# Optimization experiments

Measured on AMD Instinct MI355X. Metric: run time of the kernel, lower is better.

## Reference

```python
import jax, jax.numpy as jnp
import numpy as np
from jax import lax

B, H, W = 2, 128, 128
C_FEAT, DIM_LOI, DIM_FC = 256, 128, 1024
N_PTS0, N_PTS1 = 32, 8
L_LINES = 16384
TOPK = 300            # n_dyn_junc
JUNC_TH = 0.008       # junc_thresh
IMG_W, IMG_H = 512.0, 512.0  # annotation width/height -> sx=sy=4


def setup_inputs() -> dict:
    key = jax.random.key(0)
    ks = jax.random.split(key, 12)
    s = 0.02
    return {
        "output": jax.random.normal(ks[0], (B, 9, H, W), jnp.float32),
        "features": jax.random.normal(ks[1], (B, C_FEAT, H, W), jnp.float32),
        "line_preds": jax.random.uniform(ks[2], (B, L_LINES, 4), jnp.float32) * (W - 1),
        "conv_w": jax.random.normal(ks[3], (DIM_LOI, C_FEAT), jnp.float32) * s,
        "conv_b": jax.random.normal(ks[4], (DIM_LOI,), jnp.float32) * s,
        "w1": jax.random.normal(ks[5], (DIM_LOI * N_PTS1, DIM_FC), jnp.float32) * s,
        "b1": jax.random.normal(ks[6], (DIM_FC,), jnp.float32) * s,
        "w2": jax.random.normal(ks[7], (DIM_FC, DIM_FC), jnp.float32) * s,
        "b2": jax.random.normal(ks[8], (DIM_FC,), jnp.float32) * s,
        "w3": jax.random.normal(ks[9], (DIM_FC, 1), jnp.float32) * s,
        "b3": jax.random.normal(ks[10], (1,), jnp.float32) * s,
    }


def _nms2d(a):
    # F.max_pool2d(a, 3, stride=1, padding=1); keep only local maxima
    ap = lax.reduce_window(a, -jnp.inf, lax.max, (3, 3), (1, 1), "SAME")
    return a * (a == ap).astype(a.dtype)


def _get_junctions(jloc_nms, joff):
    # jloc_nms: [H,W]; joff: [2,H,W]
    flat = jloc_nms.reshape(-1)
    scores, idx = lax.top_k(flat, TOPK)            # [J]
    joff_f = joff.reshape(2, -1)
    y = (idx // W).astype(jnp.float32) + joff_f[1][idx] + 0.5
    x = (idx % W).astype(jnp.float32) + joff_f[0][idx] + 0.5
    juncs = jnp.stack([x, y], axis=-1)             # [J,2]
    valid = scores > JUNC_TH
    juncs = jnp.where(valid[:, None], juncs, 1e6)
    return juncs, valid


def _pool_lines(feat, lines, w1, b1, w2, b2, w3, b3):
    # feat: [C,H,W]; lines: [L,4] (x1,y1,x2,y2)
    C = feat.shape[0]
    L = lines.shape[0]
    t = jnp.linspace(0.0, 1.0, N_PTS0)                       # tspan
    start, end = lines[:, :2], lines[:, 2:]
    # [L, n_pts0, 2] sample points along each line
    pts = start[:, None, :] * t[None, :, None] + end[:, None, :] * (1.0 - t)[None, :, None] - 0.5
    px = pts[..., 0].reshape(-1)
    py = pts[..., 1].reshape(-1)
    px0 = jnp.clip(jnp.floor(px), 0.0, W - 1.0)
    py0 = jnp.clip(jnp.floor(py), 0.0, H - 1.0)
    px1 = jnp.clip(px0 + 1.0, 0.0, W - 1.0)
    py1 = jnp.clip(py0 + 1.0, 0.0, H - 1.0)
    x0, y0 = px0.astype(jnp.int32), py0.astype(jnp.int32)
    x1, y1 = px1.astype(jnp.int32), py1.astype(jnp.int32)
    f2 = feat.reshape(C, H * W)

    def g(yi, xi):
        return f2[:, yi * W + xi]                             # [C, L*n_pts0]

    xp = (g(y0, x0) * (py1 - py) * (px1 - px)
          + g(y1, x0) * (py - py0) * (px1 - px)
          + g(y0, x1) * (py1 - py) * (px - px0)
          + g(y1, x1) * (py - py0) * (px - px0))
    xp = xp.reshape(C, L, N_PTS0).transpose(1, 0, 2)          # [L, C, n_pts0]
    # MaxPool1d(kernel=n_pts0//n_pts1, stride same)
    xp = xp.reshape(L, C, N_PTS1, N_PTS0 // N_PTS1).max(-1)   # [L, C, n_pts1]
    xp = xp.reshape(L, C * N_PTS1)
    h = jax.nn.relu(xp @ w1 + b1)
    h = jax.nn.relu(h @ w2 + b2)
    return (h @ w3 + b3).ravel()                              # [L]


def _per_image(out9, loi_feat, lines_prop, w1, b1, w2, b2, w3, b3):
    jloc = jax.nn.softmax(out9[5:7], axis=0)[1]               # [H,W]
    joff = jax.nn.sigmoid(out9[7:9]) - 0.5                    # [2,H,W]
    juncs, _ = _get_junctions(_nms2d(jloc), joff)             # [J,2]
    # nearest junction to each line endpoint
    d1 = jnp.sum((lines_prop[None, :, :2] - juncs[:, None]) ** 2, axis=-1)  # [J,L]
    d2 = jnp.sum((lines_prop[None, :, 2:] - juncs[:, None]) ** 2, axis=-1)
    i1 = jnp.argmin(d1, axis=0)
    i2 = jnp.argmin(d2, axis=0)
    imin = jnp.minimum(i1, i2)
    imax = jnp.maximum(i1, i2)
    iskeep = imin < imax                                      # drop degenerate
    lines = jnp.concatenate([juncs[imin], juncs[imax]], axis=1)  # [L,4]
    logits = _pool_lines(loi_feat, lines, w1, b1, w2, b2, w3, b3)
    scores = jax.nn.sigmoid(logits)
    keep = iskeep & (scores > 0.05)
    sx = IMG_W / W
    sy = IMG_H / H
    lines2 = lines.reshape(-1, 2, 2) * jnp.array([sx, sy], jnp.float32)
    return lines2, scores, keep


def reference(output, features, line_preds, conv_w, conv_b, w1, b1, w2, b2, w3, b3):
    # 1x1 conv: dim_feat -> dim_loi
    loi = jnp.einsum("bchw,dc->bdhw", features, conv_w) + conv_b[None, :, None, None]
    fn = lambda o, f, lp: _per_image(o, f, lp, w1, b1, w2, b2, w3, b3)
    lines, scores, keep = jax.vmap(fn)(output, loi, line_preds)
    return lines, scores, keep
```

## Files before the change

kernel.cpp:

```cpp
#include <hip/hip_runtime.h>
#include <hip/hip_bf16.h>
#include <cstdint>
#include <cstddef>

#define HW     16384
#define WIDTH  128
#define NB     2
#define NTOPK  300
#define JUNC_TH 0.008f

typedef __attribute__((ext_vector_type(8))) short s16x8;
typedef __attribute__((ext_vector_type(2))) float f32x2;
typedef __attribute__((ext_vector_type(4))) float f32x4;
typedef __attribute__((ext_vector_type(4))) int   i32x4;
typedef __attribute__((ext_vector_type(8))) int   i32x8;

__device__ __forceinline__ float sigm(float x) { return 1.0f / (1.0f + expf(-x)); }

__device__ __forceinline__ unsigned short f2bf(float f) {
  __hip_bfloat16 h = __float2bfloat16(f);
  return __hip_bfloat16_raw(h).x;
}
__device__ __forceinline__ unsigned char f2fp8(float v) {
  return (unsigned char)(__builtin_amdgcn_cvt_pk_fp8_f32(v, 0.0f, 0, false) & 0xff);
}
__device__ __forceinline__ f32x2 bfpair(unsigned int u) {
  f32x2 r;
  r[0] = __uint_as_float(u << 16);
  r[1] = __uint_as_float(u & 0xffff0000u);
  return r;
}
__device__ __forceinline__ f32x2 pkmul(f32x2 a, f32x2 b) {
  f32x2 d;
  asm("v_pk_mul_f32 %0, %1, %2" : "=v"(d) : "v"(a), "v"(b));
  return d;
}
__device__ __forceinline__ f32x2 pkadd(f32x2 a, f32x2 b) {
  f32x2 d;
  asm("v_pk_add_f32 %0, %1, %2" : "=v"(d) : "v"(a), "v"(b));
  return d;
}
__device__ __forceinline__ f32x2 max2(f32x2 a, f32x2 b) {
  f32x2 r;
  r[0] = fmaxf(a[0], b[0]);
  r[1] = fmaxf(a[1], b[1]);
  return r;
}

#define GLOAD_LDS16(gp, lp)                                                        \
  __builtin_amdgcn_global_load_lds((const __attribute__((address_space(1))) void*)(gp), \
                                   (__attribute__((address_space(3))) void*)(lp), 16, 0, 0)

__device__ __forceinline__ void fc_tile_map(int bid, int nm, int& m_idx, int& n_idx) {
  if ((nm & 7) == 0) {
    int x = bid & 7;
    int k = bid >> 3;
    m_idx = x * (nm >> 3) + (k >> 2);
    n_idx = k & 3;
  } else {
    m_idx = bid >> 2;
    n_idx = bid & 3;
  }
}

__global__ void k_transpose_w(const float* __restrict__ w, float* __restrict__ wt) {
  int i = blockIdx.x * 256 + threadIdx.x;
  int d = i & 127, c = i >> 7;
  wt[c * 128 + d] = w[d * 256 + c];
}

__global__ __launch_bounds__(256) void k_wtrans(const float* __restrict__ w,
                                                unsigned char* __restrict__ wt) {
  __shared__ float tile[32][33];
  int n0 = blockIdx.x * 32, k0 = blockIdx.y * 32;
  int tx = threadIdx.x & 31, ty = threadIdx.x >> 5;
#pragma unroll
  for (int r = 0; r < 32; r += 8)
    tile[ty + r][tx] = w[(size_t)(k0 + ty + r) * 1024 + n0 + tx];
  __syncthreads();
#pragma unroll
  for (int r = 0; r < 32; r += 8)
    wt[(size_t)(n0 + ty + r) * 1024 + k0 + tx] = f2fp8(tile[tx][ty + r]);
}

__global__ __launch_bounds__(256) void k_loi(const float* __restrict__ F,
                                             const float* __restrict__ wt,
                                             const float* __restrict__ bias,
                                             unsigned short* __restrict__ loi) {
  int b = blockIdx.y;
  int p0 = blockIdx.x * 64;
  __shared__ float As[8][64];
  __shared__ float Bs[8][128];
  int t = threadIdx.x;
  int tn = t & 15;
  int tm = t >> 4;
  float acc[4][8];
#pragma unroll
  for (int i = 0; i < 4; ++i)
#pragma unroll
    for (int j = 0; j < 8; ++j) acc[i][j] = 0.0f;

  const float* Fb = F + (size_t)b * 256 * HW;
  for (int c0 = 0; c0 < 256; c0 += 8) {
    __syncthreads();
    if (t < 128) {
      int kk = t >> 4, mv = t & 15;
      float4 v = *(const float4*)(Fb + (size_t)(c0 + kk) * HW + p0 + mv * 4);
      *(float4*)&As[kk][mv * 4] = v;
    }
    {
      int kk = t >> 5, dv = t & 31;
      float4 v = *(const float4*)(wt + (size_t)(c0 + kk) * 128 + dv * 4);
      *(float4*)&Bs[kk][dv * 4] = v;
    }
    __syncthreads();
#pragma unroll
    for (int kk = 0; kk < 8; ++kk) {
      float4 a4 = *(const float4*)&As[kk][tm * 4];
      float4 b0 = *(const float4*)&Bs[kk][tn * 8];
      float4 b1 = *(const float4*)&Bs[kk][tn * 8 + 4];
      float av[4] = {a4.x, a4.y, a4.z, a4.w};
      float bv[8] = {b0.x, b0.y, b0.z, b0.w, b1.x, b1.y, b1.z, b1.w};
#pragma unroll
      for (int i = 0; i < 4; ++i)
#pragma unroll
        for (int j = 0; j < 8; ++j) acc[i][j] += av[i] * bv[j];
    }
  }
  float4 c0v = *(const float4*)(bias + tn * 8);
  float4 c1v = *(const float4*)(bias + tn * 8 + 4);
  float bb[8] = {c0v.x, c0v.y, c0v.z, c0v.w, c1v.x, c1v.y, c1v.z, c1v.w};
#pragma unroll
  for (int i = 0; i < 4; ++i) {
    int p = p0 + tm * 4 + i;
    alignas(16) unsigned short o[8];
#pragma unroll
    for (int j = 0; j < 8; ++j) o[j] = f2bf(acc[i][j] + bb[j]);
    *(s16x8*)(loi + ((size_t)b * HW + p) * 128 + tn * 8) = *(const s16x8*)o;
  }
}

__global__ void k_jloc(const float* __restrict__ out9, float* __restrict__ jloc) {
  int i = blockIdx.x * 256 + threadIdx.x;
  int b = i >> 14, p = i & (HW - 1);
  const float* base = out9 + (size_t)b * 9 * HW;
  float o5 = base[5 * HW + p], o6 = base[6 * HW + p];
  float m = fmaxf(o5, o6);
  float e5 = expf(o5 - m), e6 = expf(o6 - m);
  jloc[i] = e6 / (e5 + e6);
}

__global__ void k_nmskey(const float* __restrict__ jloc, unsigned long long* __restrict__ keys) {
  int i = blockIdx.x * 256 + threadIdx.x;
  int b = i >> 14, p = i & (HW - 1);
  int y = p >> 7, x = p & 127;
  const float* J = jloc + (size_t)b * HW;
  float c = J[p];
  float m = c;
  for (int dy = -1; dy <= 1; ++dy) {
    int yy = y + dy;
    if (yy < 0 || yy > 127) continue;
    for (int dx = -1; dx <= 1; ++dx) {
      int xx = x + dx;
      if (xx < 0 || xx > 127) continue;
      m = fmaxf(m, J[yy * WIDTH + xx]);
    }
  }
  unsigned int vb = (c == m) ? __float_as_uint(c) : 0u;
  keys[i] = ((unsigned long long)vb << 32) | (unsigned int)(~p);
}

__global__ __launch_bounds__(1024) void k_topk(const unsigned long long* __restrict__ keys,
                                               const float* __restrict__ out9,
                                               float* __restrict__ jx, float* __restrict__ jy) {
  int b = blockIdx.x;
  __shared__ unsigned long long cand[4096];
  __shared__ int cnt;
  int t = threadIdx.x;
  if (t == 0) cnt = 0;
#pragma unroll
  for (int i = t; i < 4096; i += 1024) cand[i] = 0ull;
  __syncthreads();
  const unsigned long long* K = keys + (size_t)b * HW;
  for (int i = t; i < HW; i += 1024) {
    unsigned long long k = K[i];
    if ((k >> 32) != 0ull) {
      int pos = atomicAdd(&cnt, 1);
      if (pos < 4096) cand[pos] = k;
    }
  }
  __syncthreads();
  for (int k = 2; k <= 4096; k <<= 1) {
    for (int j = k >> 1; j > 0; j >>= 1) {
#pragma unroll
      for (int idx = t; idx < 4096; idx += 1024) {
        int ixj = idx ^ j;
        if (ixj > idx) {
          unsigned long long a = cand[idx], c = cand[ixj];
          bool up = ((idx & k) == 0);
          if (up ? (a < c) : (a > c)) { cand[idx] = c; cand[ixj] = a; }
        }
      }
      __syncthreads();
    }
  }
  if (t < NTOPK) {
    const float* o7 = out9 + (size_t)b * 9 * HW + 7 * HW;
    const float* o8 = out9 + (size_t)b * 9 * HW + 8 * HW;
    unsigned long long bb = cand[t];
    unsigned int vb = (unsigned int)(bb >> 32);
    float val = __uint_as_float(vb);
    if (vb != 0u && val > JUNC_TH) {
      int p = (int)(~((unsigned int)(bb & 0xffffffffull))) & (HW - 1);
      float ox = sigm(o7[p]) - 0.5f;
      float oy = sigm(o8[p]) - 0.5f;
      jx[b * NTOPK + t] = (float)(p & 127) + ox + 0.5f;
      jy[b * NTOPK + t] = (float)(p >> 7) + oy + 0.5f;
    } else {
      jx[b * NTOPK + t] = 1000000.0f;
      jy[b * NTOPK + t] = 1000000.0f;
    }
  }
}

__global__ __launch_bounds__(256) void k_lines(const float* __restrict__ lp,
                                               const float* __restrict__ jx,
                                               const float* __restrict__ jy,
                                               float4* __restrict__ lines4,
                                               int* __restrict__ iskeep,
                                               float* __restrict__ out_lines) {
  int b = blockIdx.y;
  int l = blockIdx.x * 256 + threadIdx.x;
  __shared__ float jxs[NTOPK], jys[NTOPK];
  for (int i = threadIdx.x; i < NTOPK; i += 256) {
    jxs[i] = jx[b * NTOPK + i];
    jys[i] = jy[b * NTOPK + i];
  }
  __syncthreads();
  int gl = b * HW + l;
  const float* L = lp + (size_t)gl * 4;
  float x1 = L[0], y1 = L[1], x2 = L[2], y2 = L[3];
  float bd1 = 3.4e38f, bd2 = 3.4e38f;
  int i1 = 0, i2 = 0;
  for (int j = 0; j < NTOPK; ++j) {
    float ax = __fsub_rn(x1, jxs[j]);
    float ay = __fsub_rn(y1, jys[j]);
    float d1 = __fadd_rn(__fmul_rn(ax, ax), __fmul_rn(ay, ay));
    if (d1 < bd1) { bd1 = d1; i1 = j; }
    float ex = __fsub_rn(x2, jxs[j]);
    float ey = __fsub_rn(y2, jys[j]);
    float d2 = __fadd_rn(__fmul_rn(ex, ex), __fmul_rn(ey, ey));
    if (d2 < bd2) { bd2 = d2; i2 = j; }
  }
  int imin = min(i1, i2), imax = max(i1, i2);
  float sx1 = jxs[imin], sy1 = jys[imin], sx2 = jxs[imax], sy2 = jys[imax];
  lines4[gl] = make_float4(sx1, sy1, sx2, sy2);
  iskeep[gl] = (imin < imax) ? 1 : 0;
  ((float4*)out_lines)[gl] = make_float4(sx1 * 4.0f, sy1 * 4.0f, sx2 * 4.0f, sy2 * 4.0f);
}

__global__ __launch_bounds__(128) void k_sample(const unsigned short* __restrict__ loi,
                                                const float4* __restrict__ lines4,
                                                unsigned char* __restrict__ xvec,
                                                int b_base, int l0, int rows_per_b) {
  __shared__ __align__(16) int   soff[2][32][4];
  __shared__ __align__(16) f32x2 swt2[2][32][4];
  int b = b_base + blockIdx.y;
  int t = threadIdx.x;
  if (t < 64) {
    int li = t >> 5, k = t & 31;
    int l = l0 + blockIdx.x * 2 + li;
    float4 ln = lines4[b * HW + l];
    float tt = (float)k * (1.0f / 31.0f);
    float tc = 1.0f - tt;
    float px = ln.x * tt + ln.z * tc - 0.5f;
    float py = ln.y * tt + ln.w * tc - 0.5f;
    float px0 = fminf(fmaxf(floorf(px), 0.0f), 127.0f);
    float py0 = fminf(fmaxf(floorf(py), 0.0f), 127.0f);
    float px1 = fminf(px0 + 1.0f, 127.0f);
    float py1 = fminf(py0 + 1.0f, 127.0f);
    int ix0 = (int)px0, iy0 = (int)py0, ix1 = (int)px1, iy1 = (int)py1;
    float wy1 = __fsub_rn(py1, py), wy0 = __fsub_rn(py, py0);
    float wx1 = __fsub_rn(px1, px), wx0 = __fsub_rn(px, px0);
    soff[li][k][0] = (iy0 * WIDTH + ix0) * 128;
    soff[li][k][1] = (iy1 * WIDTH + ix0) * 128;
    soff[li][k][2] = (iy0 * WIDTH + ix1) * 128;
    soff[li][k][3] = (iy1 * WIDTH + ix1) * 128;
    float wa = __fmul_rn(wy1, wx1);
    float wb = __fmul_rn(wy0, wx1);
    float wc = __fmul_rn(wy1, wx0);
    float wd = __fmul_rn(wy0, wx0);
    swt2[li][k][0] = (f32x2){wa, wa};
    swt2[li][k][1] = (f32x2){wb, wb};
    swt2[li][k][2] = (f32x2){wc, wc};
    swt2[li][k][3] = (f32x2){wd, wd};
  }
  __syncthreads();
  int li = t >> 6, c2 = t & 63;
  int l = l0 + blockIdx.x * 2 + li;
  const unsigned short* Lb = loi + (size_t)b * HW * 128 + (c2 << 1);
  f32x2 rm = (f32x2){-3.4e38f, -3.4e38f};
  f32x2 fv2[8];
#pragma unroll 4
  for (int k = 0; k < 32; ++k) {
    int4  o   = *(const int4*)soff[li][k];
    f32x4 w01 = *(const f32x4*)&swt2[li][k][0];
    f32x4 w23 = *(const f32x4*)&swt2[li][k][2];
    f32x2 wa; wa[0] = w01[0]; wa[1] = w01[1];
    f32x2 wb; wb[0] = w01[2]; wb[1] = w01[3];
    f32x2 wc; wc[0] = w23[0]; wc[1] = w23[1];
    f32x2 wd; wd[0] = w23[2]; wd[1] = w23[3];
    unsigned int u0 = *(const unsigned int*)(Lb + o.x);
    unsigned int u1 = *(const unsigned int*)(Lb + o.y);
    unsigned int u2 = *(const unsigned int*)(Lb + o.z);
    unsigned int u3 = *(const unsigned int*)(Lb + o.w);
    f32x2 s = pkadd(pkadd(pkadd(pkmul(bfpair(u0), wa), pkmul(bfpair(u1), wb)),
                          pkmul(bfpair(u2), wc)), pkmul(bfpair(u3), wd));
    rm = max2(rm, s);
    if ((k & 3) == 3) {
      fv2[k >> 2] = rm;
      rm = (f32x2){-3.4e38f, -3.4e38f};
    }
  }
  int4 pk;
  int d;
  d = __builtin_amdgcn_cvt_pk_fp8_f32(fv2[0][0], fv2[1][0], 0, false);
  d = __builtin_amdgcn_cvt_pk_fp8_f32(fv2[2][0], fv2[3][0], d, true);
  pk.x = d;
  d = __builtin_amdgcn_cvt_pk_fp8_f32(fv2[4][0], fv2[5][0], 0, false);
  d = __builtin_amdgcn_cvt_pk_fp8_f32(fv2[6][0], fv2[7][0], d, true);
  pk.y = d;
  d = __builtin_amdgcn_cvt_pk_fp8_f32(fv2[0][1], fv2[1][1], 0, false);
  d = __builtin_amdgcn_cvt_pk_fp8_f32(fv2[2][1], fv2[3][1], d, true);
  pk.z = d;
  d = __builtin_amdgcn_cvt_pk_fp8_f32(fv2[4][1], fv2[5][1], 0, false);
  d = __builtin_amdgcn_cvt_pk_fp8_f32(fv2[6][1], fv2[7][1], d, true);
  pk.w = d;
  size_t xrow = (size_t)blockIdx.y * rows_per_b + (l - l0);
  *(int4*)(xvec + xrow * 1024 + c2 * 16) = pk;
}

#define ACC_COLS(X, mi) X(mi,0) X(mi,1) X(mi,2) X(mi,3) X(mi,4) X(mi,5) X(mi,6) X(mi,7)
#define ACC_ALL(X) ACC_COLS(X,0) ACC_COLS(X,1) ACC_COLS(X,2) ACC_COLS(X,3)
#define MXMFMA(a, b, c) \
  __builtin_amdgcn_mfma_scale_f32_16x16x128_f8f6f4(a, b, c, 0, 0, 0, 0x7f7f7f7f, 0, 0x7f7f7f7f)

__device__ __forceinline__ i32x8 ldf(const unsigned char* p, int s0, int s1) {
  i32x4 lo = *(const i32x4*)(p + s0);
  i32x4 hi = *(const i32x4*)(p + s1);
  i32x8 r;
  r[0] = lo[0]; r[1] = lo[1]; r[2] = lo[2]; r[3] = lo[3];
  r[4] = hi[0]; r[5] = hi[1]; r[6] = hi[2]; r[7] = hi[3];
  return r;
}

template <int MODE>
__global__ __launch_bounds__(512, 1) void k_fc(const unsigned char* __restrict__ A,
                                               const unsigned char* __restrict__ Bt,
                                               const float* __restrict__ bias,
                                               unsigned char* __restrict__ C,
                                               const float* __restrict__ w3,
                                               float* __restrict__ logp,
                                               int base, int nm) {
  __shared__ __align__(16) unsigned char sm[131072];
  int t = threadIdx.x, lane = t & 63, w = t >> 6;
  int wm = w & 3, wn = w >> 2;
  int lr = lane & 15, ls = lane >> 4;
  int m_idx, n_idx;
  fc_tile_map(blockIdx.x, nm, m_idx, n_idx);
  int m0 = m_idx * 256, n0 = n_idx * 256;

  int srow = t >> 3;
  int cst = (t & 7) ^ (srow & 7);
  const unsigned char* gA = A + (size_t)(m0 + srow) * 1024 + cst * 16;
  const unsigned char* gB = Bt + (size_t)(n0 + srow) * 1024 + cst * 16;
  unsigned char* sdst = sm + t * 16;

  int s0 = ((2 * ls) ^ (lr & 7)) * 16;
  int s1 = ((2 * ls + 1) ^ (lr & 7)) * 16;
  int aoff = (wm * 64 + lr) * 128;
  int boff = 32768 + (wn * 128 + lr) * 128;

#define DECLC(mi, ni) f32x4 c##mi##ni = (f32x4){0.f, 0.f, 0.f, 0.f};
  ACC_ALL(DECLC)
#undef DECLC

#pragma unroll
  for (int q = 0; q < 4; ++q) GLOAD_LDS16(gA + (size_t)q * 65536, sdst + q * 8192);
#pragma unroll
  for (int q = 0; q < 4; ++q) GLOAD_LDS16(gB + (size_t)q * 65536, sdst + 32768 + q * 8192);
  __syncthreads();

#pragma unroll 2
  for (int it = 0; it < 8; ++it) {
    int cur = it & 1;
    if (it < 7) {
      int kb = (it + 1) * 128;
      unsigned char* d = sdst + (cur ^ 1) * 65536;
#pragma unroll
      for (int q = 0; q < 4; ++q) GLOAD_LDS16(gA + kb + (size_t)q * 65536, d + q * 8192);
#pragma unroll
      for (int q = 0; q < 4; ++q) GLOAD_LDS16(gB + kb + (size_t)q * 65536, d + 32768 + q * 8192);
    }
    const unsigned char* T = sm + cur * 65536;
    const unsigned char* TA = T + aoff;
    const unsigned char* TB = T + boff;
    i32x8 a0 = ldf(TA, s0, s1);
    i32x8 a1 = ldf(TA + 2048, s0, s1);
    i32x8 a2 = ldf(TA + 4096, s0, s1);
    i32x8 a3 = ldf(TA + 6144, s0, s1);
#define DO_NI(ni)                                    \
    {                                                \
      i32x8 b_ = ldf(TB + ni * 2048, s0, s1);        \
      c0##ni = MXMFMA(a0, b_, c0##ni);               \
      c1##ni = MXMFMA(a1, b_, c1##ni);               \
      c2##ni = MXMFMA(a2, b_, c2##ni);               \
      c3##ni = MXMFMA(a3, b_, c3##ni);               \
    }
    DO_NI(0) DO_NI(1) DO_NI(2) DO_NI(3) DO_NI(4) DO_NI(5) DO_NI(6) DO_NI(7)
#undef DO_NI
    __syncthreads();
  }

#define DECLBV(ni) float bv##ni = bias[n0 + wn * 128 + ni * 16 + lr];
  DECLBV(0) DECLBV(1) DECLBV(2) DECLBV(3) DECLBV(4) DECLBV(5) DECLBV(6) DECLBV(7)
#undef DECLBV

  if constexpr (MODE == 0) {
    __syncthreads();
#define EPI(mi, ni)                                                          \
    {                                                                        \
      int cl = wn * 128 + ni * 16 + lr;                                      \
      int rl = wm * 64 + mi * 16 + ls * 4;                                   \
      sm[(rl + 0) * 272 + cl] = f2fp8(fmaxf(c##mi##ni[0] + bv##ni, 0.0f));   \
      sm[(rl + 1) * 272 + cl] = f2fp8(fmaxf(c##mi##ni[1] + bv##ni, 0.0f));   \
      sm[(rl + 2) * 272 + cl] = f2fp8(fmaxf(c##mi##ni[2] + bv##ni, 0.0f));   \
      sm[(rl + 3) * 272 + cl] = f2fp8(fmaxf(c##mi##ni[3] + bv##ni, 0.0f));   \
    }
    ACC_ALL(EPI)
#undef EPI
    __syncthreads();
#pragma unroll
    for (int p = 0; p < 8; ++p) {
      int row = p * 32 + (t >> 4), seg = t & 15;
      *(int4*)(C + (size_t)(m0 + row) * 1024 + n0 + seg * 16) =
          *(const int4*)(sm + row * 272 + seg * 16);
    }
  } else {
#define DECLWV(ni) float wv##ni = w3[n0 + wn * 128 + ni * 16 + lr];
    DECLWV(0) DECLWV(1) DECLWV(2) DECLWV(3) DECLWV(4) DECLWV(5) DECLWV(6) DECLWV(7)
#undef DECLWV
    f32x4 pm0 = (f32x4){0.f, 0.f, 0.f, 0.f}, pm1 = pm0, pm2 = pm0, pm3 = pm0;
#define RED(mi, ni)                                                   \
    {                                                                 \
      pm##mi[0] += fmaxf(c##mi##ni[0] + bv##ni, 0.0f) * wv##ni;       \
      pm##mi[1] += fmaxf(c##mi##ni[1] + bv##ni, 0.0f) * wv##ni;       \
      pm##mi[2] += fmaxf(c##mi##ni[2] + bv##ni, 0.0f) * wv##ni;       \
      pm##mi[3] += fmaxf(c##mi##ni[3] + bv##ni, 0.0f) * wv##ni;       \
    }
    ACC_ALL(RED)
#undef RED
    __syncthreads();
    float* red = (float*)sm;
#define SHF(mi, r)                                                    \
    {                                                                 \
      float v = pm##mi[r];                                            \
      v += __shfl_xor(v, 1, 64);                                      \
      v += __shfl_xor(v, 2, 64);                                      \
      v += __shfl_xor(v, 4, 64);                                      \
      v += __shfl_xor(v, 8, 64);                                      \
      if (lr == 0) red[(wm * 64 + mi * 16 + ls * 4 + r) * 2 + wn] = v; \
    }
    SHF(0, 0) SHF(0, 1) SHF(0, 2) SHF(0, 3)
    SHF(1, 0) SHF(1, 1) SHF(1, 2) SHF(1, 3)
    SHF(2, 0) SHF(2, 1) SHF(2, 2) SHF(2, 3)
    SHF(3, 0) SHF(3, 1) SHF(3, 2) SHF(3, 3)
#undef SHF
    __syncthreads();
    if (t < 256)
      logp[(size_t)(base + m0 + t) * 4 + n_idx] = red[t * 2] + red[t * 2 + 1];
  }
}

__global__ __launch_bounds__(256) void k_fin(const float* __restrict__ logp,
                                             const float* __restrict__ b3,
                                             const int* __restrict__ iskeep,
                                             float* __restrict__ oscore,
                                             float* __restrict__ okeep,
                                             int base) {
  int gl = base + blockIdx.x * 256 + threadIdx.x;
  float4 a = ((const float4*)logp)[gl];
  float s = (a.x + a.y) + (a.z + a.w);
  float sc = sigm(s + b3[0]);
  oscore[gl] = sc;
  okeep[gl] = (iskeep[gl] && sc > 0.05f) ? 1.0f : 0.0f;
}

extern "C" void kernel_launch(void* const* d_in, const int* in_sizes, int n_in,
                              void* d_out, int out_size, void* d_ws, size_t ws_size,
                              hipStream_t stream) {
  const float* output     = (const float*)d_in[0];
  const float* features   = (const float*)d_in[1];
  const float* line_preds = (const float*)d_in[2];
  const float* conv_w     = (const float*)d_in[3];
  const float* conv_b     = (const float*)d_in[4];
  const float* w1         = (const float*)d_in[5];
  const float* b1         = (const float*)d_in[6];
  const float* w2         = (const float*)d_in[7];
  const float* b2         = (const float*)d_in[8];
  const float* w3         = (const float*)d_in[9];
  const float* b3         = (const float*)d_in[10];

  char* ws = (char*)d_ws;
  size_t off = 0;
  auto alloc = [&](size_t bytes) -> void* {
    void* p = ws + off;
    off += (bytes + 255) & ~(size_t)255;
    return p;
  };
  float* wt      = (float*)alloc((size_t)256 * 128 * 4);
  unsigned short* loi = (unsigned short*)alloc((size_t)NB * HW * 128 * 2);
  float* jloc    = (float*)alloc((size_t)NB * HW * 4);
  unsigned long long* keys = (unsigned long long*)alloc((size_t)NB * HW * 8);
  float* jx      = (float*)alloc((size_t)NB * NTOPK * 4);
  float* jy      = (float*)alloc((size_t)NB * NTOPK * 4);
  float4* lines4 = (float4*)alloc((size_t)NB * HW * 16);
  int* iskeep    = (int*)alloc((size_t)NB * HW * 4);
  float* logp    = (float*)alloc((size_t)NB * HW * 4 * 4);
  unsigned char* w1b = (unsigned char*)alloc((size_t)1024 * 1024);
  unsigned char* w2b = (unsigned char*)alloc((size_t)1024 * 1024);
  size_t fixed = off;

  bool merged = (fixed + (size_t)2 * NB * HW * 1024 + 512 <= ws_size);
  int CH = 256;
  if (!merged) {
    const int cands[7] = {16384, 8192, 4096, 2048, 1024, 512, 256};
    for (int ci = 0; ci < 7; ++ci) {
      if (fixed + (size_t)2 * cands[ci] * 1024 + 512 <= ws_size) { CH = cands[ci]; break; }
    }
  }
  size_t actrows = merged ? (size_t)NB * HW : (size_t)CH;
  unsigned char* xvec = (unsigned char*)alloc(actrows * 1024);
  unsigned char* h1   = (unsigned char*)alloc(actrows * 1024);

  float* out_lines  = (float*)d_out;
  float* out_scores = out_lines + (size_t)NB * HW * 4;
  float* out_keep   = out_scores + (size_t)NB * HW;

  k_transpose_w<<<128, 256, 0, stream>>>(conv_w, wt);
  k_wtrans<<<dim3(32, 32), 256, 0, stream>>>(w1, w1b);
  k_wtrans<<<dim3(32, 32), 256, 0, stream>>>(w2, w2b);
  k_loi<<<dim3(HW / 64, NB), 256, 0, stream>>>(features, wt, conv_b, loi);
  k_jloc<<<NB * HW / 256, 256, 0, stream>>>(output, jloc);
  k_nmskey<<<NB * HW / 256, 256, 0, stream>>>(jloc, keys);
  k_topk<<<NB, 1024, 0, stream>>>(keys, output, jx, jy);
  k_lines<<<dim3(HW / 256, NB), 256, 0, stream>>>(line_preds, jx, jy, lines4, iskeep, out_lines);

  if (merged) {
    int M = NB * HW, nm = M / 256;
    k_sample<<<dim3(HW / 2, NB), 128, 0, stream>>>(loi, lines4, xvec, 0, 0, HW);
    k_fc<0><<<nm * 4, 512, 0, stream>>>(xvec, w1b, b1, h1, nullptr, nullptr, 0, nm);
    k_fc<1><<<nm * 4, 512, 0, stream>>>(h1, w2b, b2, nullptr, w3, logp, 0, nm);
    k_fin<<<M / 256, 256, 0, stream>>>(logp, b3, iskeep, out_scores, out_keep, 0);
  } else {
    int nchunk = HW / CH, nm = CH / 256;
    for (int b = 0; b < NB; ++b) {
      for (int ci = 0; ci < nchunk; ++ci) {
        int l0 = ci * CH;
        int base = b * HW + l0;
        k_sample<<<dim3(CH / 2, 1), 128, 0, stream>>>(loi, lines4, xvec, b, l0, CH);
        k_fc<0><<<nm * 4, 512, 0, stream>>>(xvec, w1b, b1, h1, nullptr, nullptr, 0, nm);
        k_fc<1><<<nm * 4, 512, 0, stream>>>(h1, w2b, b2, nullptr, w3, logp, base, nm);
        k_fin<<<CH / 256, 256, 0, stream>>>(logp, b3, iskeep, out_scores, out_keep, base);
      }
    }
  }
}
```

Before: 333.2 us.

## Compute 1x1 conv projection with bf16 MFMA instead of scalar FMA

Rewrites the k_loi 1x1-convolution GEMM so that features and weights are converted to bf16 while staged in shared memory, and the products run on the MFMA 16x16x32 bf16 instruction with fp32 accumulation. The K step grows from 8 to 32 channels per iteration. This removes the scalar FP32 FMA loop. In exchange it lowers input precision to bf16, and the transposed staging uses scalar shared-memory stores plus narrow 2-byte scattered output writes.

```diff
diff --git a/kernel.cpp b/kernel.cpp
--- a/kernel.cpp
+++ b/kernel.cpp
@@ -87,56 +87,72 @@
                                              const float* __restrict__ wt,
                                              const float* __restrict__ bias,
                                              unsigned short* __restrict__ loi) {
+  __shared__ __align__(16) unsigned short Ash[64 * 40];
+  __shared__ __align__(16) unsigned short Bsh[128 * 40];
   int b = blockIdx.y;
   int p0 = blockIdx.x * 64;
-  __shared__ float As[8][64];
-  __shared__ float Bs[8][128];
   int t = threadIdx.x;
-  int tn = t & 15;
-  int tm = t >> 4;
-  float acc[4][8];
-#pragma unroll
-  for (int i = 0; i < 4; ++i)
-#pragma unroll
-    for (int j = 0; j < 8; ++j) acc[i][j] = 0.0f;
-
+  int wv = t >> 6, lane = t & 63;
+  int lr = lane & 15, ls = lane >> 4;
   const float* Fb = F + (size_t)b * 256 * HW;
-  for (int c0 = 0; c0 < 256; c0 += 8) {
-    __syncthreads();
-    if (t < 128) {
-      int kk = t >> 4, mv = t & 15;
-      float4 v = *(const float4*)(Fb + (size_t)(c0 + kk) * HW + p0 + mv * 4);
-      *(float4*)&As[kk][mv * 4] = v;
-    }
-    {
-      int kk = t >> 5, dv = t & 31;
-      float4 v = *(const float4*)(wt + (size_t)(c0 + kk) * 128 + dv * 4);
-      *(float4*)&Bs[kk][dv * 4] = v;
-    }
-    __syncthreads();
-#pragma unroll
-    for (int kk = 0; kk < 8; ++kk) {
-      float4 a4 = *(const float4*)&As[kk][tm * 4];
-      float4 b0 = *(const float4*)&Bs[kk][tn * 8];
-      float4 b1 = *(const float4*)&Bs[kk][tn * 8 + 4];
-      float av[4] = {a4.x, a4.y, a4.z, a4.w};
-      float bv[8] = {b0.x, b0.y, b0.z, b0.w, b1.x, b1.y, b1.z, b1.w};
-#pragma unroll
-      for (int i = 0; i < 4; ++i)
-#pragma unroll
-        for (int j = 0; j < 8; ++j) acc[i][j] += av[i] * bv[j];
-    }
-  }
-  float4 c0v = *(const float4*)(bias + tn * 8);
-  float4 c1v = *(const float4*)(bias + tn * 8 + 4);
-  float bb[8] = {c0v.x, c0v.y, c0v.z, c0v.w, c1v.x, c1v.y, c1v.z, c1v.w};
-#pragma unroll
-  for (int i = 0; i < 4; ++i) {
-    int p = p0 + tm * 4 + i;
-    alignas(16) unsigned short o[8];
-#pragma unroll
-    for (int j = 0; j < 8; ++j) o[j] = f2bf(acc[i][j] + bb[j]);
-    *(s16x8*)(loi + ((size_t)b * HW + p) * 128 + tn * 8) = *(const s16x8*)o;
+
+  f32x4 acc[8];
+#pragma unroll
+  for (int dg = 0; dg < 8; ++dg) acc[dg] = (f32x4){0.f, 0.f, 0.f, 0.f};
+
+  int cc = t >> 3, pg = t & 7;
+
+  for (int c0 = 0; c0 < 256; c0 += 32) {
+    const float* fr = Fb + (size_t)(c0 + cc) * HW + p0 + pg * 8;
+    float4 fa0 = *(const float4*)fr;
+    float4 fa1 = *(const float4*)(fr + 4);
+    const float* wr = wt + (size_t)(c0 + cc) * 128 + pg * 16;
+    float4 fb0 = *(const float4*)wr;
+    float4 fb1 = *(const float4*)(wr + 4);
+    float4 fb2 = *(const float4*)(wr + 8);
+    float4 fb3 = *(const float4*)(wr + 12);
+    __syncthreads();
+    Ash[(pg * 8 + 0) * 40 + cc] = f2bf(fa0.x);
+    Ash[(pg * 8 + 1) * 40 + cc] = f2bf(fa0.y);
+    Ash[(pg * 8 + 2) * 40 + cc] = f2bf(fa0.z);
+    Ash[(pg * 8 + 3) * 40 + cc] = f2bf(fa0.w);
+    Ash[(pg * 8 + 4) * 40 + cc] = f2bf(fa1.x);
+    Ash[(pg * 8 + 5) * 40 + cc] = f2bf(fa1.y);
+    Ash[(pg * 8 + 6) * 40 + cc] = f2bf(fa1.z);
+    Ash[(pg * 8 + 7) * 40 + cc] = f2bf(fa1.w);
+    Bsh[(pg * 16 +  0) * 40 + cc] = f2bf(fb0.x);
+    Bsh[(pg * 16 +  1) * 40 + cc] = f2bf(fb0.y);
+    Bsh[(pg * 16 +  2) * 40 + cc] = f2bf(fb0.z);
+    Bsh[(pg * 16 +  3) * 40 + cc] = f2bf(fb0.w);
+    Bsh[(pg * 16 +  4) * 40 + cc] = f2bf(fb1.x);
+    Bsh[(pg * 16 +  5) * 40 + cc] = f2bf(fb1.y);
+    Bsh[(pg * 16 +  6) * 40 + cc] = f2bf(fb1.z);
+    Bsh[(pg * 16 +  7) * 40 + cc] = f2bf(fb1.w);
+    Bsh[(pg * 16 +  8) * 40 + cc] = f2bf(fb2.x);
+    Bsh[(pg * 16 +  9) * 40 + cc] = f2bf(fb2.y);
+    Bsh[(pg * 16 + 10) * 40 + cc] = f2bf(fb2.z);
+    Bsh[(pg * 16 + 11) * 40 + cc] = f2bf(fb2.w);
+    Bsh[(pg * 16 + 12) * 40 + cc] = f2bf(fb3.x);
+    Bsh[(pg * 16 + 13) * 40 + cc] = f2bf(fb3.y);
+    Bsh[(pg * 16 + 14) * 40 + cc] = f2bf(fb3.z);
+    Bsh[(pg * 16 + 15) * 40 + cc] = f2bf(fb3.w);
+    __syncthreads();
+    s16x8 av = *(const s16x8*)&Ash[(wv * 16 + lr) * 40 + ls * 8];
+#pragma unroll
+    for (int dg = 0; dg < 8; ++dg) {
+      s16x8 bv = *(const s16x8*)&Bsh[(dg * 16 + lr) * 40 + ls * 8];
+      acc[dg] = __builtin_amdgcn_mfma_f32_16x16x32_bf16(av, bv, acc[dg], 0, 0, 0);
+    }
+  }
+#pragma unroll
+  for (int dg = 0; dg < 8; ++dg) {
+    int d = dg * 16 + lr;
+    float bb = bias[d];
+#pragma unroll
+    for (int r = 0; r < 4; ++r) {
+      int p = p0 + wv * 16 + ls * 4 + r;
+      loi[((size_t)b * HW + p) * 128 + d] = f2bf(acc[dg][r] + bb);
+    }
   }
 }
 
```

Result: faster. 314.7 us (-5.6%).
